# Kernel tuning notes

Measured on AMD Instinct MI355X. Metric: run time of the kernel, lower is better.

## Reference

```python
import jax, jax.numpy as jnp
import numpy as np

NUM_ENTITIES = 100000
NUM_TIMES = 10000
D = 512
DB = 768
NUM_REL = 200
NUM_BASES = 4
N_NODES = 30000
N_EDGES = 200000
B = 128
P_ENT = 64
P_TIME = 32
T_UNIQ = 2000


def setup_inputs() -> dict:
    key = jax.random.key(0)
    ks = jax.random.split(key, 32)
    n = jax.random.normal
    ri = jax.random.randint
    inp = {}
    # learned params
    inp['emb'] = n(ks[0], (NUM_ENTITIES + NUM_TIMES, D), jnp.float32) * 0.05
    sc = 1.0 / np.sqrt(D)
    inp['basis1'] = n(ks[1], (NUM_BASES, D, D), jnp.float32) * sc
    inp['att1'] = n(ks[2], (NUM_REL, NUM_BASES), jnp.float32) * 0.5
    inp['root1'] = n(ks[3], (D, D), jnp.float32) * sc
    inp['bias1'] = jnp.zeros((D,), jnp.float32)
    inp['basis2'] = n(ks[4], (NUM_BASES, D, D), jnp.float32) * sc
    inp['att2'] = n(ks[5], (NUM_REL, NUM_BASES), jnp.float32) * 0.5
    inp['root2'] = n(ks[6], (D, D), jnp.float32) * sc
    inp['bias2'] = jnp.zeros((D,), jnp.float32)
    sb = 1.0 / np.sqrt(DB)
    inp['W_lin'] = n(ks[7], (DB, D), jnp.float32) * sb
    inp['b_lin'] = jnp.zeros((D,), jnp.float32)
    inp['W_attn'] = n(ks[8], (DB, D), jnp.float32) * sb
    inp['b_attn'] = jnp.zeros((D,), jnp.float32)
    inp['W_prob'] = n(ks[9], (DB, 1), jnp.float32) * sb
    inp['b_prob'] = jnp.zeros((1,), jnp.float32)
    # forward tensor args
    inp['ques_emb_bert'] = n(ks[10], (B, DB), jnp.float32)
    inp['x_idx'] = ri(ks[11], (N_NODES,), 0, NUM_ENTITIES, jnp.int32)
    inp['edge_index'] = ri(ks[12], (2, N_EDGES), 0, N_NODES, jnp.int32)
    inp['edge_type'] = ri(ks[13], (N_EDGES,), 0, NUM_REL, jnp.int32)
    inp['start_time'] = ri(ks[14], (N_EDGES,), 0, NUM_TIMES, jnp.int32)
    inp['end_time'] = ri(ks[15], (N_EDGES,), 0, NUM_TIMES, jnp.int32)
    inp['edge_batch_idx'] = jnp.sort(ri(ks[16], (N_EDGES,), 0, B, jnp.int32))
    inp['edge_norm'] = jax.random.uniform(ks[17], (N_EDGES,), jnp.float32)
    inp['uniq_times'] = ri(ks[18], (T_UNIQ,), 0, NUM_TIMES, jnp.int32)
    # padded index vectors: positions >= count point at the appended zero row
    ent_counts = ri(ks[19], (B,), 1, P_ENT + 1, jnp.int32)
    time_counts = ri(ks[20], (B,), 1, P_TIME + 1, jnp.int32)
    pe = ri(ks[21], (B, P_ENT), 0, N_NODES, jnp.int32)
    pt = ri(ks[22], (B, P_TIME), 0, T_UNIQ, jnp.int32)
    inp['padded_ent'] = jnp.where(jnp.arange(P_ENT)[None, :] < ent_counts[:, None], pe, N_NODES)
    inp['padded_time'] = jnp.where(jnp.arange(P_TIME)[None, :] < time_counts[:, None], pt, T_UNIQ)
    inp['ent_counts'] = ent_counts
    inp['time_counts'] = time_counts
    return inp


def rgcn_layer(x, basis, att, root, bias, src, dst, etype, st_emb, et_emb, q_t, edge_norm):
    # basis decomposition: project all nodes through each basis once. [N, NB, D]
    xb = jnp.einsum('ni,bio->nbo', x, basis)
    coeff = att[etype]                                 # [E, NB]
    msg = jnp.einsum('eb,ebd->ed', coeff, xb[src])     # [E, D]
    # time gate: question-time embedding vs edge interval midpoint embedding
    gate = jax.nn.sigmoid(jnp.sum(q_t * 0.5 * (st_emb + et_emb), axis=-1))  # [E]
    msg = msg * (gate * edge_norm)[:, None]
    agg = jax.ops.segment_sum(msg, dst, num_segments=N_NODES)
    return agg + x @ root + bias


def reference(emb, basis1, att1, root1, bias1, basis2, att2, root2, bias2,
              W_lin, b_lin, W_attn, b_attn, W_prob, b_prob,
              ques_emb_bert, x_idx, edge_index, edge_type, start_time, end_time,
              edge_batch_idx, edge_norm, uniq_times, padded_ent, padded_time,
              ent_counts, time_counts):
    question_embedding = ques_emb_bert @ W_lin + b_lin                  # [B, D]
    time_for_edge_attn = (ques_emb_bert @ W_attn + b_attn)[edge_batch_idx]  # [E, D]
    st_emb = emb[start_time + NUM_ENTITIES]
    et_emb = emb[end_time + NUM_ENTITIES]
    x = emb[x_idx]                                                      # [N, D]
    src, dst = edge_index[0], edge_index[1]
    h = jax.nn.relu(rgcn_layer(x, basis1, att1, root1, bias1, src, dst, edge_type,
                               st_emb, et_emb, time_for_edge_attn, edge_norm))
    # dropout is identity in eval mode
    h = rgcn_layer(h, basis2, att2, root2, bias2, src, dst, edge_type,
                   st_emb, et_emb, time_for_edge_attn, edge_norm)       # [N, D]
    subgraph_time_emb = emb[uniq_times + NUM_ENTITIES]                  # [T_u, D]
    zero = jnp.zeros((1, D), h.dtype)
    ent_w_zeros = jnp.concatenate([h, zero], axis=0)
    time_w_zeros = jnp.concatenate([subgraph_time_emb, zero], axis=0)
    pooled_ent = jnp.sum(ent_w_zeros[padded_ent], axis=1) / ent_counts[:, None].astype(h.dtype)
    pooled_time = jnp.sum(time_w_zeros[padded_time], axis=1) / time_counts[:, None].astype(h.dtype)
    p_ent = jax.nn.sigmoid(ques_emb_bert @ W_prob + b_prob)             # [B, 1]
    pred = (question_embedding + pooled_ent * p_ent + pooled_time * (1.0 - p_ent)) / 3.0
    # batched cosine similarity against full entity+time vocab
    pred_n = pred / jnp.maximum(jnp.linalg.norm(pred, axis=-1, keepdims=True), 1e-8)
    emb_n = emb / jnp.maximum(jnp.linalg.norm(emb, axis=-1, keepdims=True), 1e-8)
    score = pred_n @ emb_n.T                                            # [B, V]
    return score * 30.0
```

## Files before the change

kernel.cpp:

```cpp
#include <hip/hip_runtime.h>

#define NUM_ENT   100000
#define NTIMES    10000
#define DD        512
#define DB        768
#define NREL      200
#define NBAS      4
#define NN        30000
#define NEDGE     200000
#define BATCH     128
#define PENT      64
#define PTIME     32
#define TUNIQ     2000
#define V_TOT     110000
#define M_PAD2    30208
#define MT2R      1888
#define KT_L      80
#define KT_E      16
#define TCT       632

typedef __attribute__((ext_vector_type(8))) short s8v;
typedef __attribute__((ext_vector_type(4))) float f4v;

__device__ __forceinline__ unsigned short f2bf(float x){
  unsigned int u = __builtin_bit_cast(unsigned int, x);
  u += 0x7fffu + ((u >> 16) & 1u);
  return (unsigned short)(u >> 16);
}
__device__ __forceinline__ float bf2f(unsigned short h){
  unsigned int u = ((unsigned int)h) << 16;
  return __builtin_bit_cast(float, u);
}

__device__ __forceinline__ void gload16(const void* g, void* l){
  __builtin_amdgcn_global_load_lds(
      (const __attribute__((address_space(1))) void*)g,
      (__attribute__((address_space(3))) void*)l, 16, 0, 0);
}


__global__ __launch_bounds__(256) void k_small2(const float* __restrict__ ques,
    const float* __restrict__ Wl, const float* __restrict__ bl,
    const float* __restrict__ Wa, const float* __restrict__ ba,
    const float* __restrict__ Wp, const float* __restrict__ bp,
    float* __restrict__ qlin, float* __restrict__ qattn, float* __restrict__ pent){
  if (blockIdx.x == 32){
    int b = threadIdx.x >> 1, half = threadIdx.x & 1;
    float a = 0.f;
    int k0 = half * 384;
    for (int k = k0; k < k0 + 384; ++k)
      a = fmaf(ques[(size_t)b * DB + k], Wp[k], a);
    a += __shfl_xor(a, 1);
    if (half == 0) pent[b] = 1.f / (1.f + expf(-(a + bp[0])));
    return;
  }
  __shared__ float sq[128 * 96];
  int col = threadIdx.x & 31, bg = threadIdx.x >> 5;
  int c0 = blockIdx.x * 32;
  const float* W = (c0 < 512) ? Wl : Wa;
  int wcol = (c0 & 511) + col;
  float acc[16] = {};
  for (int k0 = 0; k0 < DB; k0 += 96){
    __syncthreads();
    for (int i = threadIdx.x; i < 128 * 96; i += 256){
      int b = i / 96, kk = i - b * 96;
      sq[i] = ques[(size_t)b * DB + k0 + kk];
    }
    __syncthreads();
    for (int kk = 0; kk < 96; kk += 4){
      float w0 = W[(size_t)(k0 + kk + 0) * 512 + wcol];
      float w1 = W[(size_t)(k0 + kk + 1) * 512 + wcol];
      float w2 = W[(size_t)(k0 + kk + 2) * 512 + wcol];
      float w3 = W[(size_t)(k0 + kk + 3) * 512 + wcol];
      #pragma unroll
      for (int bb = 0; bb < 16; ++bb){
        float4 qv = *reinterpret_cast<const float4*>(&sq[(bg * 16 + bb) * 96 + kk]);
        acc[bb] = fmaf(qv.x, w0, fmaf(qv.y, w1, fmaf(qv.z, w2, fmaf(qv.w, w3, acc[bb]))));
      }
    }
  }
  float* dst = (c0 < 512) ? qlin : qattn;
  const float* bias = (c0 < 512) ? bl : ba;
  #pragma unroll
  for (int bb = 0; bb < 16; ++bb)
    dst[(size_t)(bg * 16 + bb) * 512 + wcol] = acc[bb] + bias[wcol];
}

__global__ __launch_bounds__(256) void k_pack_qrows(const float* __restrict__ src,
    unsigned short* __restrict__ Ap){
  int w = (int)((blockIdx.x * 256 + threadIdx.x) >> 6);
  int lane = threadIdx.x & 63;
  if (w >= BATCH) return;
  const float* p = src + (size_t)w * 512 + lane * 8;
  s8v o;
  #pragma unroll
  for (int j = 0; j < 8; ++j) o[j] = (short)f2bf(p[j]);
  *reinterpret_cast<s8v*>(Ap + ((size_t)((w >> 4) * KT_E + (lane >> 2)) << 9)
                             + ((w & 15) + (lane & 3) * 16) * 8) = o;
}

__global__ __launch_bounds__(256) void k_pack_B(const float* __restrict__ basis,
    const float* __restrict__ root, unsigned short* __restrict__ Bp){
  int idx = blockIdx.x * 256 + threadIdx.x;
  if (idx >= KT_L * 32 * 64) return;
  int lane = idx & 63; int kt = idx >> 11;
  int k0 = kt * 32 + (lane >> 4) * 8;
  int col = ((idx >> 6) & 31) * 16 + (lane & 15);
  s8v o;
  #pragma unroll
  for (int j = 0; j < 8; ++j){
    int k = k0 + j;
    float v = (k < 2048) ? basis[(size_t)k * 512 + col] : root[(size_t)(k - 2048) * 512 + col];
    o[j] = (short)f2bf(v);
  }
  *reinterpret_cast<s8v*>(Bp + (size_t)idx * 8) = o;
}

__global__ __launch_bounds__(256) void k_pack_temb(const float* __restrict__ emb,
    unsigned short* __restrict__ Bt){
  int idx = blockIdx.x * 256 + threadIdx.x;
  if (idx >= KT_E * TCT * 64) return;
  int lane = idx & 63;
  int ct = (idx >> 6) % TCT;
  int kt = idx / (TCT * 64);
  int c = ct * 16 + (lane & 15);
  int k0 = kt * 32 + (lane >> 4) * 8;
  s8v o;
  if (c < NTIMES){
    const float* p = emb + (size_t)(NUM_ENT + c) * 512 + k0;
    #pragma unroll
    for (int j = 0; j < 8; ++j) o[j] = (short)f2bf(p[j]);
  } else {
    #pragma unroll
    for (int j = 0; j < 8; ++j) o[j] = 0;
  }
  *reinterpret_cast<s8v*>(Bt + (size_t)idx * 8) = o;
}

__global__ __launch_bounds__(256) void k_gemm_m2(
    const unsigned short* __restrict__ A, const unsigned short* __restrict__ B,
    float* __restrict__ outf){
  __shared__ __align__(1024) short sAll[3 * 8192];
  const int Kt = KT_E;
  int tid = threadIdx.x;
  int lane = tid & 63, wid = tid >> 6;
  int wr = wid >> 1, wc = wid & 1;
  int rt0 = blockIdx.x * 8;
  int ct0 = blockIdx.y * 8;
  const unsigned short* pA0 = A + ((size_t)(rt0 + 2 * wid) * Kt) * 512 + lane * 8;
  const unsigned short* pA1 = pA0 + (size_t)Kt * 512;
  const unsigned short* pB0 = B + (size_t)(ct0 + 2 * wid) * 512 + lane * 8;
  const unsigned short* pB1 = pB0 + 512;
  size_t gbs = (size_t)TCT * 512;
  int so = 2 * wid * 512;
  f4v acc[4][4] = {};

  auto STAGE = [&](int buf, int kt){
    short* b = &sAll[buf * 8192];
    gload16(pA0 + (size_t)kt * 512, b + so);
    gload16(pA1 + (size_t)kt * 512, b + so + 512);
    gload16(pB0 + (size_t)kt * gbs, b + 4096 + so);
    gload16(pB1 + (size_t)kt * gbs, b + 4096 + so + 512);
  };
  auto COMPUTE = [&](int buf){
    const short* base = &sAll[buf * 8192];
    s8v af[4], bfr[4];
    #pragma unroll
    for (int m = 0; m < 4; ++m) af[m] = *reinterpret_cast<const s8v*>(base + (wr * 4 + m) * 512 + lane * 8);
    #pragma unroll
    for (int n = 0; n < 4; ++n) bfr[n] = *reinterpret_cast<const s8v*>(base + 4096 + (wc * 4 + n) * 512 + lane * 8);
    #pragma unroll
    for (int m = 0; m < 4; ++m)
      #pragma unroll
      for (int n = 0; n < 4; ++n)
        acc[m][n] = __builtin_amdgcn_mfma_f32_16x16x32_bf16(af[m], bfr[n], acc[m][n], 0, 0, 0);
  };

  STAGE(0, 0);
  STAGE(1, 1);
  int cb = 0, sb = 2;
  for (int kt = 0; kt < Kt - 2; ++kt){
    STAGE(sb, kt + 2);
    asm volatile("s_waitcnt vmcnt(8)" ::: "memory");
    __builtin_amdgcn_s_barrier();
    __builtin_amdgcn_sched_barrier(0);
    COMPUTE(cb);
    __builtin_amdgcn_s_barrier();
    cb = (cb == 2) ? 0 : cb + 1;
    sb = (sb == 2) ? 0 : sb + 1;
  }
  asm volatile("s_waitcnt vmcnt(4)" ::: "memory");
  __builtin_amdgcn_s_barrier();
  __builtin_amdgcn_sched_barrier(0);
  COMPUTE(cb);
  cb = (cb == 2) ? 0 : cb + 1;
  asm volatile("s_waitcnt vmcnt(0)" ::: "memory");
  __builtin_amdgcn_s_barrier();
  __builtin_amdgcn_sched_barrier(0);
  COMPUTE(cb);

  #pragma unroll
  for (int m = 0; m < 4; ++m)
    #pragma unroll
    for (int n = 0; n < 4; ++n){
      int row0 = rt0 * 16 + (wr * 4 + m) * 16 + ((lane >> 4) * 4);
      int col  = (ct0 + wc * 4 + n) * 16 + (lane & 15);
      #pragma unroll
      for (int r = 0; r < 4; ++r){
        int rr = row0 + r;
        if (col < NTIMES) outf[(size_t)rr * NTIMES + col] = acc[m][n][r];
      }
    }
}

template<int MODE>
__global__ __launch_bounds__(512, 4) void k_gemm256(
    const unsigned short* __restrict__ A, const unsigned short* __restrict__ B,
    const float* __restrict__ bias, unsigned short* __restrict__ outh){
  __shared__ __align__(1024) short sAll[3 * 12288];
  const int Kt = KT_L;
  int tid = threadIdx.x;
  int lane = tid & 63, wid = tid >> 6;
  int wr = wid >> 1, wc = wid & 1;
  int g = blockIdx.x;
  int ng = (g & 7) * 59 + (g >> 3);
  int blkM = ng >> 2, blkN = ng & 3;
  int rt0 = blkM * 16;
  int ct0 = blkN * 8;
  const unsigned short* pA0 = A + ((size_t)(rt0 + wid) * Kt) * 512 + lane * 8;
  const unsigned short* pA1 = A + ((size_t)(rt0 + 8 + wid) * Kt) * 512 + lane * 8;
  const unsigned short* pB0 = B + (size_t)(ct0 + wid) * 512 + lane * 8;
  const size_t gbs = 32 * 512;
  int soA0 = wid * 512, soA1 = (8 + wid) * 512, soB = 8192 + wid * 512;
  f4v acc[4][4] = {};

  auto STAGE = [&](int buf, int kt){
    short* b = &sAll[buf * 12288];
    gload16(pA0 + (size_t)kt * 512, b + soA0);
    gload16(pA1 + (size_t)kt * 512, b + soA1);
    gload16(pB0 + (size_t)kt * gbs, b + soB);
  };
  auto COMPUTE = [&](int buf){
    const short* base = &sAll[buf * 12288];
    s8v af[4], bfr[4];
    #pragma unroll
    for (int m = 0; m < 4; ++m) af[m] = *reinterpret_cast<const s8v*>(base + (wr * 4 + m) * 512 + lane * 8);
    #pragma unroll
    for (int n = 0; n < 4; ++n) bfr[n] = *reinterpret_cast<const s8v*>(base + 8192 + (wc * 4 + n) * 512 + lane * 8);
    __builtin_amdgcn_s_setprio(1);
    #pragma unroll
    for (int m = 0; m < 4; ++m)
      #pragma unroll
      for (int n = 0; n < 4; ++n)
        acc[m][n] = __builtin_amdgcn_mfma_f32_16x16x32_bf16(af[m], bfr[n], acc[m][n], 0, 0, 0);
    __builtin_amdgcn_s_setprio(0);
  };

  STAGE(0, 0);
  STAGE(1, 1);
  int cb = 0, sb = 2;
  for (int kt = 0; kt < Kt - 2; ++kt){
    STAGE(sb, kt + 2);
    asm volatile("s_waitcnt vmcnt(6)" ::: "memory");
    __builtin_amdgcn_s_barrier();
    __builtin_amdgcn_sched_barrier(0);
    COMPUTE(cb);
    __builtin_amdgcn_s_barrier();
    cb = (cb == 2) ? 0 : cb + 1;
    sb = (sb == 2) ? 0 : sb + 1;
  }
  asm volatile("s_waitcnt vmcnt(3)" ::: "memory");
  __builtin_amdgcn_s_barrier();
  __builtin_amdgcn_sched_barrier(0);
  COMPUTE(cb);
  cb = (cb == 2) ? 0 : cb + 1;
  asm volatile("s_waitcnt vmcnt(0)" ::: "memory");
  __builtin_amdgcn_s_barrier();
  __builtin_amdgcn_sched_barrier(0);
  COMPUTE(cb);

  int R0 = blkM * 256 + wr * 64 + (lane >> 4) * 4;
  int C0 = blkN * 128 + wc * 64 + (lane & 15);
  #pragma unroll
  for (int m = 0; m < 4; ++m)
    #pragma unroll
    for (int n = 0; n < 4; ++n){
      int col = C0 + n * 16;
      float bb = bias[col];
      #pragma unroll
      for (int r4 = 0; r4 < 4; ++r4){
        int rr = R0 + m * 16 + r4;
        if (rr < NN){
          float v = acc[m][n][r4] + bb;
          if constexpr (MODE == 1) v = fmaxf(v, 0.f);
          outh[(size_t)rr * 512 + col] = f2bf(v);
        }
      }
    }
}

__global__ __launch_bounds__(256) void k_edgeprep(const int* __restrict__ ebatch,
    const int* __restrict__ st, const int* __restrict__ et,
    const float* __restrict__ enorm, const float* __restrict__ M2,
    const int* __restrict__ ei,
    float* __restrict__ we, int* __restrict__ cnt, int* __restrict__ lists){
  int e = blockIdx.x * 256 + threadIdx.x;
  if (e >= NEDGE) return;
  int b = ebatch[e];
  float s = 0.5f * (M2[(size_t)b * NTIMES + st[e]] + M2[(size_t)b * NTIMES + et[e]]);
  we[e] = (1.f / (1.f + expf(-s))) * enorm[e];
  int dst = ei[NEDGE + e];
  int slot = atomicAdd(&cnt[dst], 1);
  if (slot < 64) lists[(size_t)dst * 64 + slot] = e;
}

__global__ __launch_bounds__(256) void k_gather_x(const int* __restrict__ x_idx,
    const float* __restrict__ emb, unsigned short* __restrict__ Ap,
    unsigned short* __restrict__ x_rm){
  int w = (int)((blockIdx.x * 256 + threadIdx.x) >> 6);
  int lane = threadIdx.x & 63;
  if (w >= NN) return;
  int v = x_idx[w];
  const float4* p = reinterpret_cast<const float4*>(emb + (size_t)v * 512 + lane * 8);
  float4 a = p[0], b = p[1];
  s8v x;
  x[0] = (short)f2bf(a.x); x[1] = (short)f2bf(a.y); x[2] = (short)f2bf(a.z); x[3] = (short)f2bf(a.w);
  x[4] = (short)f2bf(b.x); x[5] = (short)f2bf(b.y); x[6] = (short)f2bf(b.z); x[7] = (short)f2bf(b.w);
  *reinterpret_cast<s8v*>(x_rm + (size_t)w * 512 + lane * 8) = x;
  *reinterpret_cast<s8v*>(Ap + ((size_t)(w >> 4) * KT_L + 64 + (lane >> 2)) * 512
                             + ((w & 15) + (lane & 3) * 16) * 8) = x;
}

__global__ __launch_bounds__(256) void k_pack_rows(const unsigned short* __restrict__ src_rm,
    unsigned short* __restrict__ Ap){
  int w = (int)((blockIdx.x * 256 + threadIdx.x) >> 6);
  int lane = threadIdx.x & 63;
  if (w >= NN) return;
  s8v x = *reinterpret_cast<const s8v*>(src_rm + (size_t)w * 512 + lane * 8);
  *reinterpret_cast<s8v*>(Ap + ((size_t)(w >> 4) * KT_L + 64 + (lane >> 2)) * 512
                             + ((w & 15) + (lane & 3) * 16) * 8) = x;
}

__global__ __launch_bounds__(256) void k_edge_agg(const unsigned short* __restrict__ xsrc,
    const int* __restrict__ ei, const int* __restrict__ etype,
    const float* __restrict__ we, const float* __restrict__ att,
    const int* __restrict__ cnt, const int* __restrict__ lists,
    unsigned short* __restrict__ Ap){
  __shared__ float satt[NREL * NBAS];
  __shared__ int sed[4][64];
  for (int i = threadIdx.x; i < NREL * NBAS; i += 256) satt[i] = att[i];
  int wid = threadIdx.x >> 6, lane = threadIdx.x & 63;
  int n = blockIdx.x * 4 + wid;
  int deg = min(cnt[n], 64);
  int eid = (lane < deg) ? lists[(size_t)n * 64 + lane] : 0x7fffffff;
  int rank = 0;
  for (int j = 0; j < 64; ++j){
    int v = __shfl(eid, j);
    rank += (v < eid) ? 1 : 0;
  }
  __syncthreads();
  if (lane < deg) sed[wid][rank] = eid;
  __syncthreads();
  float acc[NBAS][8] = {};
  if (deg > 0){
    int my_e = sed[wid][(lane < deg) ? lane : 0];
    int my_s = ei[my_e];
    int my_t = etype[my_e];
    float my_w = we[my_e];
    float c0l = my_w * satt[my_t * 4 + 0];
    float c1l = my_w * satt[my_t * 4 + 1];
    float c2l = my_w * satt[my_t * 4 + 2];
    float c3l = my_w * satt[my_t * 4 + 3];
    int s0 = __shfl(my_s, 0);
    s8v xv = *reinterpret_cast<const s8v*>(xsrc + (size_t)s0 * 512 + lane * 8);
    for (int j = 0; j < deg; ++j){
      s8v xn = xv;
      if (j + 1 < deg){
        int sn = __shfl(my_s, j + 1);
        xn = *reinterpret_cast<const s8v*>(xsrc + (size_t)sn * 512 + lane * 8);
      }
      float c0 = __shfl(c0l, j), c1 = __shfl(c1l, j);
      float c2 = __shfl(c2l, j), c3 = __shfl(c3l, j);
      #pragma unroll
      for (int jj = 0; jj < 8; ++jj){
        float x = bf2f((unsigned short)xv[jj]);
        acc[0][jj] = fmaf(c0, x, acc[0][jj]);
        acc[1][jj] = fmaf(c1, x, acc[1][jj]);
        acc[2][jj] = fmaf(c2, x, acc[2][jj]);
        acc[3][jj] = fmaf(c3, x, acc[3][jj]);
      }
      xv = xn;
    }
  }
  #pragma unroll
  for (int b = 0; b < NBAS; ++b){
    s8v o;
    #pragma unroll
    for (int jj = 0; jj < 8; ++jj) o[jj] = (short)f2bf(acc[b][jj]);
    *reinterpret_cast<s8v*>(Ap + ((size_t)(n >> 4) * KT_L + b * 16 + (lane >> 2)) * 512
                               + ((n & 15) + (lane & 3) * 16) * 8) = o;
  }
}

__global__ __launch_bounds__(256) void k_pred(const unsigned short* __restrict__ h2,
    const float* __restrict__ emb, const int* __restrict__ uniq,
    const int* __restrict__ pent_idx, const int* __restrict__ ptime_idx,
    const int* __restrict__ ent_c, const int* __restrict__ time_c,
    const float* __restrict__ qlin, const float* __restrict__ pent,
    unsigned short* __restrict__ Ap_pred){
  __shared__ float sacc[4][512];
  int b = blockIdx.x;
  int wid = threadIdx.x >> 6, lane = threadIdx.x & 63;
  float a[8] = {};
  if (wid < 2){
    for (int j = wid * 32; j < wid * 32 + 32; ++j){
      int idx = pent_idx[b * PENT + j];
      if (idx < NN){
        s8v hv = *reinterpret_cast<const s8v*>(h2 + (size_t)idx * 512 + lane * 8);
        #pragma unroll
        for (int jj = 0; jj < 8; ++jj) a[jj] += bf2f((unsigned short)hv[jj]);
      }
    }
  } else {
    for (int j = (wid - 2) * 16; j < (wid - 2) * 16 + 16; ++j){
      int ti = ptime_idx[b * PTIME + j];
      if (ti < TUNIQ){
        const float* p = emb + (size_t)(NUM_ENT + uniq[ti]) * 512 + lane * 8;
        #pragma unroll
        for (int jj = 0; jj < 8; ++jj) a[jj] += p[jj];
      }
    }
  }
  #pragma unroll
  for (int jj = 0; jj < 8; ++jj) sacc[wid][lane * 8 + jj] = a[jj];
  __syncthreads();
  if (wid == 0){
    float ce = 1.f / (float)ent_c[b], ct = 1.f / (float)time_c[b];
    float p = pent[b];
    float pr[8]; float ss = 0.f;
    #pragma unroll
    for (int jj = 0; jj < 8; ++jj){
      int i = lane * 8 + jj;
      float ae = sacc[0][i] + sacc[1][i];
      float at = sacc[2][i] + sacc[3][i];
      float v = (qlin[(size_t)b * 512 + i] + ae * ce * p + at * ct * (1.f - p)) * (1.f / 3.f);
      pr[jj] = v; ss += v * v;
    }
    ss += __shfl_xor(ss, 32); ss += __shfl_xor(ss, 16); ss += __shfl_xor(ss, 8);
    ss += __shfl_xor(ss, 4);  ss += __shfl_xor(ss, 2);  ss += __shfl_xor(ss, 1);
    float inv = 1.f / fmaxf(sqrtf(ss), 1e-8f);
    s8v o;
    #pragma unroll
    for (int jj = 0; jj < 8; ++jj) o[jj] = (short)f2bf(pr[jj] * inv);
    *reinterpret_cast<s8v*>(Ap_pred + ((size_t)((b >> 4) * KT_E + (lane >> 2)) << 9)
                                    + ((b & 15) + (lane & 3) * 16) * 8) = o;
  }
}

__global__ __launch_bounds__(512) void k_score(
    const unsigned short* __restrict__ Apred, const float* __restrict__ emb,
    float* __restrict__ out){
  __shared__ __align__(1024) short sA[2][4096];
  __shared__ __align__(1024) short sB[2][8192];
  __shared__ float sf[512];
  int tid = threadIdx.x;
  int lane = tid & 63, wid = tid >> 6;
  int wr = wid >> 2, wc = wid & 3;
  int c0 = blockIdx.x * 256;
  int bc = tid & 255;
  int kh = tid >> 8;
  int col_l = bc;
  int colg = c0 + col_l;
  bool cval = colg < V_TOT;
  const float* gB = emb + (size_t)colg * 512 + kh * 16;
  int ctl = bc >> 4;
  int wb0 = ctl * 512 + ((2 * kh + 0) * 16 + (bc & 15)) * 8;
  int wb1 = wb0 + 128;
  const unsigned short* gA = Apred + ((size_t)wid * KT_E) * 512 + lane * 8;
  float ss = 0.f;
  float4 q0, q1, q2, q3;
  f4v acc[4][4] = {};

  auto LOADB = [&](int s){
    if (cval){
      const float4* p = reinterpret_cast<const float4*>(gB + s * 32);
      q0 = p[0]; q1 = p[1]; q2 = p[2]; q3 = p[3];
    } else {
      q0 = q1 = q2 = q3 = float4{0.f, 0.f, 0.f, 0.f};
    }
  };
  auto WRITEB = [&](int p){
    short* bb = &sB[p][0];
    s8v o0, o1;
    o0[0] = (short)f2bf(q0.x); o0[1] = (short)f2bf(q0.y); o0[2] = (short)f2bf(q0.z); o0[3] = (short)f2bf(q0.w);
    o0[4] = (short)f2bf(q1.x); o0[5] = (short)f2bf(q1.y); o0[6] = (short)f2bf(q1.z); o0[7] = (short)f2bf(q1.w);
    o1[0] = (short)f2bf(q2.x); o1[1] = (short)f2bf(q2.y); o1[2] = (short)f2bf(q2.z); o1[3] = (short)f2bf(q2.w);
    o1[4] = (short)f2bf(q3.x); o1[5] = (short)f2bf(q3.y); o1[6] = (short)f2bf(q3.z); o1[7] = (short)f2bf(q3.w);
    ss += q0.x*q0.x + q0.y*q0.y + q0.z*q0.z + q0.w*q0.w;
    ss += q1.x*q1.x + q1.y*q1.y + q1.z*q1.z + q1.w*q1.w;
    ss += q2.x*q2.x + q2.y*q2.y + q2.z*q2.z + q2.w*q2.w;
    ss += q3.x*q3.x + q3.y*q3.y + q3.z*q3.z + q3.w*q3.w;
    *reinterpret_cast<s8v*>(bb + wb0) = o0;
    *reinterpret_cast<s8v*>(bb + wb1) = o1;
  };
  auto COMPUTE = [&](int p){
    s8v af[4], bfr[4];
    #pragma unroll
    for (int m = 0; m < 4; ++m) af[m] = *reinterpret_cast<const s8v*>(&sA[p][(wr * 4 + m) * 512 + lane * 8]);
    #pragma unroll
    for (int n = 0; n < 4; ++n) bfr[n] = *reinterpret_cast<const s8v*>(&sB[p][(wc * 4 + n) * 512 + lane * 8]);
    #pragma unroll
    for (int m = 0; m < 4; ++m)
      #pragma unroll
      for (int n = 0; n < 4; ++n)
        acc[m][n] = __builtin_amdgcn_mfma_f32_16x16x32_bf16(af[m], bfr[n], acc[m][n], 0, 0, 0);
  };

  LOADB(0);
  gload16(gA, &sA[0][wid * 512]);
  for (int s = 0; s < 16; ++s){
    int p = s & 1;
    WRITEB(p);
    __syncthreads();
    if (s < 15){
      LOADB(s + 1);
      gload16(gA + (size_t)(s + 1) * 512, &sA[p ^ 1][wid * 512]);
    }
    COMPUTE(p);
    __syncthreads();
  }
  sf[tid] = ss;
  __syncthreads();

  int R0 = wr * 64 + (lane >> 4) * 4;
  int C0l = wc * 64 + (lane & 15);
  #pragma unroll
  for (int n = 0; n < 4; ++n){
    int cl = C0l + n * 16;
    int col = c0 + cl;
    float s2 = sf[cl] + sf[cl + 256];
    float inv = (1.f / fmaxf(sqrtf(s2), 1e-8f)) * 30.0f;
    if (col < V_TOT){
      #pragma unroll
      for (int m = 0; m < 4; ++m)
        #pragma unroll
        for (int r4 = 0; r4 < 4; ++r4){
          int rr = R0 + m * 16 + r4;
          out[(size_t)rr * V_TOT + col] = acc[m][n][r4] * inv;
        }
    }
  }
}

extern "C" void kernel_launch(void* const* d_in, const int* in_sizes, int n_in,
                              void* d_out, int out_size, void* d_ws, size_t ws_size,
                              hipStream_t stream){
  const float* emb    = (const float*)d_in[0];
  const float* basis1 = (const float*)d_in[1];
  const float* att1   = (const float*)d_in[2];
  const float* root1  = (const float*)d_in[3];
  const float* bias1  = (const float*)d_in[4];
  const float* basis2 = (const float*)d_in[5];
  const float* att2   = (const float*)d_in[6];
  const float* root2  = (const float*)d_in[7];
  const float* bias2  = (const float*)d_in[8];
  const float* W_lin  = (const float*)d_in[9];
  const float* b_lin  = (const float*)d_in[10];
  const float* W_attn = (const float*)d_in[11];
  const float* b_attn = (const float*)d_in[12];
  const float* W_prob = (const float*)d_in[13];
  const float* b_prob = (const float*)d_in[14];
  const float* ques   = (const float*)d_in[15];
  const int* x_idx    = (const int*)d_in[16];
  const int* eidx     = (const int*)d_in[17];
  const int* etype    = (const int*)d_in[18];
  const int* stime    = (const int*)d_in[19];
  const int* etime    = (const int*)d_in[20];
  const int* ebatch   = (const int*)d_in[21];
  const float* enorm  = (const float*)d_in[22];
  const int* uniq     = (const int*)d_in[23];
  const int* pent_i   = (const int*)d_in[24];
  const int* ptime_i  = (const int*)d_in[25];
  const int* ent_c    = (const int*)d_in[26];
  const int* time_c   = (const int*)d_in[27];
  float* out = (float*)d_out;

  char* w = (char*)d_ws;
  size_t off = 0;
  auto alloc = [&](size_t bytes)->char*{ char* p = w + off; off += (bytes + 255) & ~(size_t)255; return p; };
  unsigned short* Ap   = (unsigned short*)alloc((size_t)MT2R * KT_L * 1024);
  unsigned short* B1p  = (unsigned short*)alloc((size_t)KT_L * 32 * 1024);
  unsigned short* B2p  = (unsigned short*)alloc((size_t)KT_L * 32 * 1024);
  unsigned short* Bt   = (unsigned short*)alloc((size_t)KT_E * TCT * 1024);
  char* xh_base = alloc((size_t)NN * 512 * 2 * 2);
  unsigned short* x_rm = (unsigned short*)xh_base;
  unsigned short* h1   = (unsigned short*)(xh_base + (size_t)NN * 512 * 2);
  unsigned short* h2   = (unsigned short*)xh_base;
  float* M2    = (float*)alloc((size_t)BATCH * NTIMES * 4);
  float* we    = (float*)alloc((size_t)NEDGE * 4);
  float* qlin  = (float*)alloc((size_t)BATCH * 512 * 4);
  float* qattn = (float*)alloc((size_t)BATCH * 512 * 4);
  float* pent  = (float*)alloc(1024);
  unsigned short* Apq    = (unsigned short*)alloc((size_t)8 * KT_E * 1024);
  unsigned short* Appred = (unsigned short*)alloc((size_t)8 * KT_E * 1024);
  int* cnt   = (int*)alloc((size_t)NN * 4);
  int* lists = (int*)alloc((size_t)NN * 64 * 4);
  (void)ws_size; (void)in_sizes; (void)n_in; (void)out_size;

  k_small2<<<33, 256, 0, stream>>>(ques, W_lin, b_lin, W_attn, b_attn, W_prob, b_prob,
                                   qlin, qattn, pent);
  k_pack_qrows<<<32, 256, 0, stream>>>(qattn, Apq);
  k_pack_B<<<(KT_L * 32 * 64 + 255) / 256, 256, 0, stream>>>(basis1, root1, B1p);
  k_pack_B<<<(KT_L * 32 * 64 + 255) / 256, 256, 0, stream>>>(basis2, root2, B2p);
  k_pack_temb<<<(KT_E * TCT * 64) / 256, 256, 0, stream>>>(emb, Bt);
  k_gemm_m2<<<dim3(1, 79), 256, 0, stream>>>(Apq, Bt, M2);
  hipMemsetAsync(cnt, 0, (size_t)NN * 4, stream);
  k_edgeprep<<<(NEDGE + 255) / 256, 256, 0, stream>>>(ebatch, stime, etime, enorm, M2,
                                                      eidx, we, cnt, lists);
  k_gather_x<<<NN / 4, 256, 0, stream>>>(x_idx, emb, Ap, x_rm);
  k_edge_agg<<<NN / 4, 256, 0, stream>>>(x_rm, eidx, etype, we, att1, cnt, lists, Ap);
  k_gemm256<1><<<472, 512, 0, stream>>>(Ap, B1p, bias1, h1);
  k_pack_rows<<<NN / 4, 256, 0, stream>>>(h1, Ap);
  k_edge_agg<<<NN / 4, 256, 0, stream>>>(h1, eidx, etype, we, att2, cnt, lists, Ap);
  k_gemm256<2><<<472, 512, 0, stream>>>(Ap, B2p, bias2, h2);
  k_pred<<<BATCH, 256, 0, stream>>>(h2, emb, uniq, pent_i, ptime_i, ent_c, time_c,
                                    qlin, pent, Appred);
  k_score<<<430, 512, 0, stream>>>(Appred, emb, out);
}
```

Measured before the change: 719.3 us.

## Shrink score kernel tiles, read A fragments from global, reorder epilogue stores

```diff
diff --git a/kernel.cpp b/kernel.cpp
--- a/kernel.cpp
+++ b/kernel.cpp
@@ -284,14 +284,13 @@
   #pragma unroll
   for (int m = 0; m < 4; ++m)
     #pragma unroll
-    for (int n = 0; n < 4; ++n){
-      int col = C0 + n * 16;
-      float bb = bias[col];
-      #pragma unroll
-      for (int r4 = 0; r4 < 4; ++r4){
-        int rr = R0 + m * 16 + r4;
-        if (rr < NN){
-          float v = acc[m][n][r4] + bb;
+    for (int r4 = 0; r4 < 4; ++r4){
+      int rr = R0 + m * 16 + r4;
+      if (rr < NN){
+        #pragma unroll
+        for (int n = 0; n < 4; ++n){
+          int col = C0 + n * 16;
+          float v = acc[m][n][r4] + bias[col];
           if constexpr (MODE == 1) v = fmaxf(v, 0.f);
           outh[(size_t)rr * 512 + col] = f2bf(v);
         }
@@ -457,33 +456,29 @@
   }
 }
 
-__global__ __launch_bounds__(512) void k_score(
+__global__ __launch_bounds__(256, 3) void k_score(
     const unsigned short* __restrict__ Apred, const float* __restrict__ emb,
     float* __restrict__ out){
-  __shared__ __align__(1024) short sA[2][4096];
-  __shared__ __align__(1024) short sB[2][8192];
-  __shared__ float sf[512];
+  __shared__ __align__(1024) short sB[2][4096];
+  __shared__ float sf[256];
   int tid = threadIdx.x;
   int lane = tid & 63, wid = tid >> 6;
-  int wr = wid >> 2, wc = wid & 3;
-  int c0 = blockIdx.x * 256;
-  int bc = tid & 255;
-  int kh = tid >> 8;
-  int col_l = bc;
-  int colg = c0 + col_l;
+  int wr = wid >> 1, wc = wid & 1;
+  int c0 = blockIdx.x * 128;
+  int bc = tid & 127;
+  int kh = tid >> 7;
+  int colg = c0 + bc;
   bool cval = colg < V_TOT;
   const float* gB = emb + (size_t)colg * 512 + kh * 16;
-  int ctl = bc >> 4;
-  int wb0 = ctl * 512 + ((2 * kh + 0) * 16 + (bc & 15)) * 8;
+  int wb0 = (bc >> 4) * 512 + ((2 * kh) * 16 + (bc & 15)) * 8;
   int wb1 = wb0 + 128;
-  const unsigned short* gA = Apred + ((size_t)wid * KT_E) * 512 + lane * 8;
   float ss = 0.f;
   float4 q0, q1, q2, q3;
   f4v acc[4][4] = {};
 
   auto LOADB = [&](int s){
     if (cval){
-      const float4* p = reinterpret_cast<const float4*>(gB + s * 32);
+      const float4* p = reinterpret_cast<const float4*>(gB + (size_t)s * 32);
       q0 = p[0]; q1 = p[1]; q2 = p[2]; q3 = p[3];
     } else {
       q0 = q1 = q2 = q3 = float4{0.f, 0.f, 0.f, 0.f};
@@ -503,12 +498,15 @@
     *reinterpret_cast<s8v*>(bb + wb0) = o0;
     *reinterpret_cast<s8v*>(bb + wb1) = o1;
   };
-  auto COMPUTE = [&](int p){
+  auto COMPUTE = [&](int p, int s){
     s8v af[4], bfr[4];
     #pragma unroll
-    for (int m = 0; m < 4; ++m) af[m] = *reinterpret_cast<const s8v*>(&sA[p][(wr * 4 + m) * 512 + lane * 8]);
-    #pragma unroll
-    for (int n = 0; n < 4; ++n) bfr[n] = *reinterpret_cast<const s8v*>(&sB[p][(wc * 4 + n) * 512 + lane * 8]);
+    for (int m = 0; m < 4; ++m)
+      af[m] = *reinterpret_cast<const s8v*>(
+          Apred + (((size_t)(wr * 4 + m) * KT_E + s) << 9) + lane * 8);
+    #pragma unroll
+    for (int n = 0; n < 4; ++n)
+      bfr[n] = *reinterpret_cast<const s8v*>(&sB[p][(wc * 4 + n) * 512 + lane * 8]);
     #pragma unroll
     for (int m = 0; m < 4; ++m)
       #pragma unroll
@@ -517,16 +515,12 @@
   };
 
   LOADB(0);
-  gload16(gA, &sA[0][wid * 512]);
   for (int s = 0; s < 16; ++s){
     int p = s & 1;
     WRITEB(p);
     __syncthreads();
-    if (s < 15){
-      LOADB(s + 1);
-      gload16(gA + (size_t)(s + 1) * 512, &sA[p ^ 1][wid * 512]);
-    }
-    COMPUTE(p);
+    if (s < 15) LOADB(s + 1);
+    COMPUTE(p, s);
     __syncthreads();
   }
   sf[tid] = ss;
@@ -534,22 +528,29 @@
 
   int R0 = wr * 64 + (lane >> 4) * 4;
   int C0l = wc * 64 + (lane & 15);
+  float inv[4];
   #pragma unroll
   for (int n = 0; n < 4; ++n){
     int cl = C0l + n * 16;
-    int col = c0 + cl;
-    float s2 = sf[cl] + sf[cl + 256];
-    float inv = (1.f / fmaxf(sqrtf(s2), 1e-8f)) * 30.0f;
-    if (col < V_TOT){
-      #pragma unroll
-      for (int m = 0; m < 4; ++m)
+    float s2 = sf[cl] + sf[cl + 128];
+    inv[n] = (1.f / fmaxf(sqrtf(s2), 1e-8f)) * 30.0f;
+  }
+  bool cok = (c0 + 127) < V_TOT;
+  #pragma unroll
+  for (int m = 0; m < 4; ++m)
+    #pragma unroll
+    for (int r4 = 0; r4 < 4; ++r4){
+      int rr = R0 + m * 16 + r4;
+      float* orow = out + (size_t)rr * V_TOT + c0 + C0l;
+      if (cok){
         #pragma unroll
-        for (int r4 = 0; r4 < 4; ++r4){
-          int rr = R0 + m * 16 + r4;
-          out[(size_t)rr * V_TOT + col] = acc[m][n][r4] * inv;
-        }
-    }
-  }
+        for (int n = 0; n < 4; ++n) orow[n * 16] = acc[m][n][r4] * inv[n];
+      } else {
+        #pragma unroll
+        for (int n = 0; n < 4; ++n)
+          if (c0 + C0l + n * 16 < V_TOT) orow[n * 16] = acc[m][n][r4] * inv[n];
+      }
+    }
 }
 
 extern "C" void kernel_launch(void* const* d_in, const int* in_sizes, int n_in,
@@ -625,5 +626,5 @@
   k_gemm256<2><<<472, 512, 0, stream>>>(Ap, B2p, bias2, h2);
   k_pred<<<BATCH, 256, 0, stream>>>(h2, emb, uniq, pent_i, ptime_i, ent_c, time_c,
                                     qlin, pent, Appred);
-  k_score<<<430, 512, 0, stream>>>(Appred, emb, out);
-}
+  k_score<<<860, 256, 0, stream>>>(Appred, emb, out);
+}
```

After: 713.3 us. Within noise of the previous version (-0.8%).
